# Performance work log

Hardware: AMD Instinct MI355X
Metric: run time of the kernel (lower is better)

The kernel has to match this reference:

```python
import jax, jax.numpy as jnp
import numpy as np

D = 1024
H = 16
HD = D // H

def setup_inputs() -> dict:
    key = jax.random.key(0)
    ks = jax.random.split(key, 8)
    scale = 1.0 / np.sqrt(D)
    x = jax.random.normal(ks[0], (2, 2048, D), dtype=jnp.float32)
    Wq = jax.random.uniform(ks[1], (D, D), jnp.float32, -scale, scale)
    bq = jax.random.uniform(ks[2], (D,), jnp.float32, -scale, scale)
    Wk = jax.random.uniform(ks[3], (D, D), jnp.float32, -scale, scale)
    bk = jax.random.uniform(ks[4], (D,), jnp.float32, -scale, scale)
    Wv = jax.random.uniform(ks[5], (D, D), jnp.float32, -scale, scale)
    bv = jax.random.uniform(ks[6], (D,), jnp.float32, -scale, scale)
    B = jnp.zeros((1, H, 1, 1), dtype=jnp.float32)
    return {"x": x, "Wq": Wq, "bq": bq, "Wk": Wk, "bk": bk, "Wv": Wv, "bv": bv, "B": B}

def reference(x, Wq, bq, Wk, bk, Wv, bv, B):
    bsz, seq, _ = x.shape
    def proj(W, b):
        # [b, s, D] -> [b, h, s, hd]
        y = x @ W.T + b
        return y.reshape(bsz, seq, H, HD).transpose(0, 2, 1, 3)
    q = proj(Wq, bq)
    k = proj(Wk, bk)
    v = proj(Wv, bv)
    scores = jnp.einsum('bhqd,bhkd->bhqk', q, k) / np.sqrt(HD) + B
    attn = jax.nn.softmax(scores, axis=-1)
    out = jnp.einsum('bhqk,bhkd->bhqd', attn, v)
    return out.transpose(0, 2, 1, 3).reshape(bsz, seq, D)
```

## Files before the change

kernel.cpp:

```cpp
#include <hip/hip_runtime.h>
#include <stdint.h>

typedef __attribute__((ext_vector_type(8))) short s8v;
typedef __attribute__((ext_vector_type(4))) short s4v;
typedef __attribute__((ext_vector_type(4))) float f4v;
typedef __attribute__((ext_vector_type(16))) float f16v;

#define D_DIM 1024
#define H_NUM 16
#define HD 64
#define SEQ 2048
#define BSZ 2
#define MROWS (BSZ * SEQ)
#define LOG2E 1.4426950408889634f

__device__ __forceinline__ unsigned short f2bf(float f) {
  unsigned u = __builtin_bit_cast(unsigned, f);
  u += 0x7fffu + ((u >> 16) & 1u);
  return (unsigned short)(u >> 16);
}

__device__ __forceinline__ float exp2q(float x) {
  float r;
  asm("v_exp_f32 %0, %1" : "=v"(r) : "v"(x));
  return r;
}

__device__ __forceinline__ float max3q(float a, float b, float c) {
  float r;
  asm("v_max3_f32 %0, %1, %2, %3" : "=v"(r) : "v"(a), "v"(b), "v"(c));
  return r;
}

__device__ __forceinline__ unsigned int cvtpk(float a, float b) {
  unsigned int r;
  asm("v_cvt_pk_bf16_f32 %0, %1, %2" : "=v"(r) : "v"(a), "v"(b));
  return r;
}

__device__ __forceinline__ void async16(const unsigned short* g, unsigned short* l) {
  __builtin_amdgcn_global_load_lds(
      (__attribute__((address_space(1))) unsigned int*)(uintptr_t)g,
      (__attribute__((address_space(3))) unsigned int*)l, 16, 0, 0);
}

__device__ __forceinline__ f4v mfma16(s8v a, s8v b, f4v c) {
  return __builtin_amdgcn_mfma_f32_16x16x32_bf16(a, b, c, 0, 0, 0);
}

__device__ __forceinline__ f16v mfma32(s8v a, s8v b, f16v c) {
  return __builtin_amdgcn_mfma_f32_32x32x16_bf16(a, b, c, 0, 0, 0);
}

__device__ __forceinline__ void barrier_raw() {
  __builtin_amdgcn_sched_barrier(0);
  __builtin_amdgcn_s_barrier();
  __builtin_amdgcn_sched_barrier(0);
}
#define WAITVM0() asm volatile("s_waitcnt vmcnt(0)" ::: "memory")

__global__ __launch_bounds__(256) void cvt_all(
    const float* __restrict__ x, const float* __restrict__ Wq,
    const float* __restrict__ Wk, const float* __restrict__ Wv,
    unsigned short* __restrict__ Xb, unsigned short* __restrict__ Wb) {
  const int NX = MROWS * D_DIM / 4;
  const int NW = D_DIM * D_DIM / 4;
  int i = blockIdx.x * 256 + threadIdx.x;
  const float* src;
  unsigned short* dst;
  int off;
  if (i < NX) {
    src = x; dst = Xb; off = i;
  } else if (i < NX + NW) {
    src = Wq; dst = Wb; off = i - NX;
  } else if (i < NX + 2 * NW) {
    src = Wk; dst = Wb + D_DIM * D_DIM; off = i - NX - NW;
  } else {
    src = Wv; dst = Wb + 2 * D_DIM * D_DIM; off = i - NX - 2 * NW;
  }
  f4v v = *(const f4v*)(src + (size_t)off * 4);
  s4v o;
  o[0] = (short)f2bf(v[0]);
  o[1] = (short)f2bf(v[1]);
  o[2] = (short)f2bf(v[2]);
  o[3] = (short)f2bf(v[3]);
  *(s4v*)(dst + (size_t)off * 4) = o;
}

__global__ __launch_bounds__(256) void qkv_gemm(
    const unsigned short* __restrict__ Xb, const unsigned short* __restrict__ Wb,
    const float* __restrict__ bq, const float* __restrict__ bk,
    const float* __restrict__ bv, unsigned short* __restrict__ qb,
    unsigned short* __restrict__ kb, unsigned short* __restrict__ vt) {
  __shared__ __align__(16) unsigned short At[2][128 * 32];
  __shared__ __align__(16) unsigned short Bt[2][128 * 32];

  const int z = blockIdx.z;
  const unsigned short* W = Wb + z * (D_DIM * D_DIM);
  const float* bias = (z == 0) ? bq : ((z == 1) ? bk : bv);
  const int row0 = blockIdx.x * 128;
  const int col0 = blockIdx.y * 128;
  const int t = threadIdx.x;
  const int w = t >> 6, l = t & 63;
  const int wr = w >> 1, wc = w & 1;
  const int lg = l >> 4, lc = l & 15;

  f4v acc[4][4];
#pragma unroll
  for (int m = 0; m < 4; ++m)
#pragma unroll
    for (int n = 0; n < 4; ++n) acc[m][n] = (f4v){0.f, 0.f, 0.f, 0.f};

  const int srow = t >> 2;
  const int sch = (t & 3) ^ ((t >> 3) & 3);
  const unsigned short* Asrc = Xb + (size_t)(row0 + srow) * D_DIM + sch * 8;
  const unsigned short* Bsrc = W + (size_t)(col0 + srow) * D_DIM + sch * 8;

  const int rch = lg ^ ((lc >> 1) & 3);
  const int arow = wr * 64 + lc;
  const int brow = wc * 64 + lc;

#define STAGE(b, k0)                                                        \
  do {                                                                      \
    async16(Asrc + (k0), At[b] + t * 8);                                    \
    async16(Asrc + (k0) + 64 * D_DIM, At[b] + 2048 + t * 8);                \
    async16(Bsrc + (k0), Bt[b] + t * 8);                                    \
    async16(Bsrc + (k0) + 64 * D_DIM, Bt[b] + 2048 + t * 8);                \
  } while (0)

  STAGE(0, 0);
  WAITVM0();
  barrier_raw();

  int cur = 0;
  for (int it = 0; it < 32; ++it) {
    if (it < 31) STAGE(cur ^ 1, (it + 1) * 32);
    s8v a[4], b[4];
#pragma unroll
    for (int m = 0; m < 4; ++m)
      a[m] = *(const s8v*)(At[cur] + (arow + m * 16) * 32 + rch * 8);
#pragma unroll
    for (int n = 0; n < 4; ++n)
      b[n] = *(const s8v*)(Bt[cur] + (brow + n * 16) * 32 + rch * 8);
    __builtin_amdgcn_s_setprio(1);
#pragma unroll
    for (int m = 0; m < 4; ++m)
#pragma unroll
      for (int n = 0; n < 4; ++n) acc[m][n] = mfma16(a[m], b[n], acc[m][n]);
    __builtin_amdgcn_s_setprio(0);
    WAITVM0();
    barrier_raw();
    cur ^= 1;
  }
#undef STAGE

  const float SCQ = 0.125f * LOG2E;
#pragma unroll
  for (int m = 0; m < 4; ++m) {
    const int sg0 = row0 + wr * 64 + m * 16 + 4 * lg;
    const int b = sg0 >> 11;
    const int sl0 = sg0 & (SEQ - 1);
#pragma unroll
    for (int n = 0; n < 4; ++n) {
      const int j = col0 + wc * 64 + n * 16 + lc;
      const int h = j >> 6, hd = j & 63;
      const float bs = bias[j];
      if (z == 2) {
        s4v o;
#pragma unroll
        for (int r = 0; r < 4; ++r) o[r] = (short)f2bf(acc[m][n][r] + bs);
        *(s4v*)(vt + ((size_t)(b * H_NUM + h) * HD + hd) * SEQ + sl0) = o;
      } else if (z == 0) {
#pragma unroll
        for (int r = 0; r < 4; ++r)
          qb[((size_t)(b * H_NUM + h) * SEQ + (sl0 + r)) * HD + hd] =
              f2bf((acc[m][n][r] + bs) * SCQ);
      } else {
#pragma unroll
        for (int r = 0; r < 4; ++r)
          kb[((size_t)(b * H_NUM + h) * SEQ + (sl0 + r)) * HD + hd] =
              f2bf(acc[m][n][r] + bs);
      }
    }
  }
}

__global__ __launch_bounds__(512, 4) void attn_fwd(
    const unsigned short* __restrict__ qb, const unsigned short* __restrict__ kb,
    const unsigned short* __restrict__ vt, const float* __restrict__ Bb,
    float* __restrict__ out) {
  __shared__ __align__(16) unsigned short Kl[2][2][64 * 64];
  __shared__ __align__(16) unsigned short Vl[2][2][64 * 64];

  const int bh = blockIdx.x;
  const int b = bh >> 4, h = bh & 15;
  const int q0 = blockIdx.y * 128;
  const int t = threadIdx.x, w = t >> 6, l = t & 63;
  const int ql = l & 31, hi = l >> 5;
  const int g = w >> 2;
  const int pw = w & 3;
  (void)Bb;

  const unsigned short* Q = qb + (size_t)bh * SEQ * HD;
  const unsigned short* K = kb + (size_t)bh * SEQ * HD;
  const unsigned short* V = vt + (size_t)bh * HD * SEQ;

  const int qrow = q0 + pw * 32 + ql;
  const unsigned short* Qp = Q + (size_t)qrow * HD + 8 * hi;
  s8v qf[4];
#pragma unroll
  for (int ks = 0; ks < 4; ++ks) qf[ks] = *(const s8v*)(Qp + ks * 16);

  f16v zf;
#pragma unroll
  for (int i = 0; i < 16; ++i) zf[i] = 0.f;
  f16v acc0 = zf, acc1 = zf;
  float m = -3.0e38f, thr = -3.0e38f, lsum = 0.f;

  int off0[4], off1[4];
#pragma unroll
  for (int ks = 0; ks < 4; ++ks) {
    off0[ks] = ql * 64 + (((2 * ks + hi) ^ (ql & 7)) * 8);
    off1[ks] = off0[ks] + 2048;
  }

  const int tg = t & 255;
  const int srow = tg >> 3;
  const int sc8 = (tg & 7) ^ (srow & 7);
  const unsigned short* Kst = K + (size_t)(g * 1024 + srow) * HD + sc8 * 8;
  const unsigned short* Vst = V + (size_t)srow * SEQ + g * 1024 + sc8 * 8;
  unsigned short* Kd = &Kl[g][0][tg * 8];
  unsigned short* Vd = &Vl[g][0][tg * 8];
  const int ldsw = 64 * 64;

#define STAGE_KV(bsel)                                                      \
  do {                                                                      \
    async16(Kst, Kd + (bsel) * ldsw);                                       \
    async16(Kst + 32 * HD, Kd + (bsel) * ldsw + 2048);                      \
    async16(Vst, Vd + (bsel) * ldsw);                                       \
    async16(Vst + 32 * SEQ, Vd + (bsel) * ldsw + 2048);                     \
    Kst += 64 * HD;                                                         \
    Vst += 64;                                                              \
  } while (0)

  STAGE_KV(0);
  WAITVM0();
  barrier_raw();

  int cur = 0;
  for (int kt = 0; kt < 16; ++kt) {
    if (kt < 15) STAGE_KV(cur ^ 1);

    const unsigned short* Kb_ = &Kl[g][cur][0];
    const unsigned short* Vb_ = &Vl[g][cur][0];

    f16v s0, s1;
    __builtin_amdgcn_s_setprio(1);
    {
      s8v kf0 = *(const s8v*)(Kb_ + off0[0]);
      s8v kf1 = *(const s8v*)(Kb_ + off1[0]);
      s0 = mfma32(kf0, qf[0], zf);
      s1 = mfma32(kf1, qf[0], zf);
    }
#pragma unroll
    for (int ks = 1; ks < 4; ++ks) {
      s8v kf0 = *(const s8v*)(Kb_ + off0[ks]);
      s8v kf1 = *(const s8v*)(Kb_ + off1[ks]);
      s0 = mfma32(kf0, qf[ks], s0);
      s1 = mfma32(kf1, qf[ks], s1);
    }
    __builtin_amdgcn_s_setprio(0);

    float a0 = max3q(s0[0], s0[1], s0[2]);
    float a1 = max3q(s0[3], s0[4], s0[5]);
    float a2 = max3q(s0[6], s0[7], s0[8]);
    float a3 = max3q(s0[9], s0[10], s0[11]);
    float a4 = max3q(s0[12], s0[13], s0[14]);
    float a5 = max3q(s0[15], s1[0], s1[1]);
    float a6 = max3q(s1[2], s1[3], s1[4]);
    float a7 = max3q(s1[5], s1[6], s1[7]);
    float a8 = max3q(s1[8], s1[9], s1[10]);
    float a9 = max3q(s1[11], s1[12], s1[13]);
    float b0 = max3q(a0, a1, a2);
    float b1 = max3q(a3, a4, a5);
    float b2 = max3q(a6, a7, a8);
    float b3 = max3q(a9, s1[14], s1[15]);
    float tmax = fmaxf(fmaxf(b0, b1), fmaxf(b2, b3));

    if (!__all(tmax <= thr)) {
      float tr = fmaxf(tmax, __shfl_xor(tmax, 32));
      const float mn = fmaxf(m, tr);
      const float fs = exp2q(m - mn);
      m = mn;
      thr = mn + 8.0f;
#pragma unroll
      for (int i = 0; i < 16; ++i) { acc0[i] *= fs; acc1[i] *= fs; }
      lsum *= fs;
    }

#pragma unroll
    for (int i = 0; i < 16; ++i) {
      s0[i] = exp2q(s0[i] - m);
      s1[i] = exp2q(s1[i] - m);
    }
    {
      float p0 = (s0[0] + s0[1]) + (s0[2] + s0[3]);
      float p1 = (s0[4] + s0[5]) + (s0[6] + s0[7]);
      float p2 = (s0[8] + s0[9]) + (s0[10] + s0[11]);
      float p3 = (s0[12] + s0[13]) + (s0[14] + s0[15]);
      float p4 = (s1[0] + s1[1]) + (s1[2] + s1[3]);
      float p5 = (s1[4] + s1[5]) + (s1[6] + s1[7]);
      float p6 = (s1[8] + s1[9]) + (s1[10] + s1[11]);
      float p7 = (s1[12] + s1[13]) + (s1[14] + s1[15]);
      lsum += ((p0 + p1) + (p2 + p3)) + ((p4 + p5) + (p6 + p7));
    }

    unsigned int u[16];
#pragma unroll
    for (int x = 0; x < 8; ++x) {
      u[x] = cvtpk(s0[2 * x], s0[2 * x + 1]);
      u[8 + x] = cvtpk(s1[2 * x], s1[2 * x + 1]);
    }
    s8v pb[4];
#pragma unroll
    for (int ks = 0; ks < 4; ++ks) {
      const int base = (ks >> 1) * 8 + (ks & 1) * 4;
      unsigned int x0 = u[base + 0], y0 = u[base + 2];
      unsigned int x1 = u[base + 1], y1 = u[base + 3];
      asm("v_permlane32_swap_b32 %0, %1" : "+v"(x0), "+v"(y0));
      asm("v_permlane32_swap_b32 %0, %1" : "+v"(x1), "+v"(y1));
      union { s8v v; unsigned int w[4]; } bb;
      bb.w[0] = x0; bb.w[1] = x1; bb.w[2] = y0; bb.w[3] = y1;
      pb[ks] = bb.v;
    }

    __builtin_amdgcn_s_setprio(1);
#pragma unroll
    for (int ks = 0; ks < 4; ++ks) {
      s8v vf0 = *(const s8v*)(Vb_ + off0[ks]);
      s8v vf1 = *(const s8v*)(Vb_ + off1[ks]);
      acc0 = mfma32(vf0, pb[ks], acc0);
      acc1 = mfma32(vf1, pb[ks], acc1);
    }
    __builtin_amdgcn_s_setprio(0);

    WAITVM0();
    barrier_raw();
    cur ^= 1;
  }
#undef STAGE_KV

  lsum += __shfl_xor(lsum, 32);

  float* exch = (float*)&Kl[0][0][0];
  float* mlb = (float*)&Vl[0][0][0];

  __syncthreads();
  if (g == 1) {
    float* dst = exch + ((size_t)(pw * 64 + l)) * 32;
#pragma unroll
    for (int gg = 0; gg < 4; ++gg) {
      f4v v0, v1;
#pragma unroll
      for (int r = 0; r < 4; ++r) { v0[r] = acc0[4 * gg + r]; v1[r] = acc1[4 * gg + r]; }
      *(f4v*)(dst + 4 * gg) = v0;
      *(f4v*)(dst + 16 + 4 * gg) = v1;
    }
    if (hi == 0) {
      mlb[pw * 32 + ql] = m;
      mlb[128 + pw * 32 + ql] = lsum;
    }
  }
  __syncthreads();
  if (g == 0) {
    const float mb = mlb[pw * 32 + ql];
    const float lb = mlb[128 + pw * 32 + ql];
    const float ms = fmaxf(m, mb);
    const float fa = exp2q(m - ms);
    const float fb = exp2q(mb - ms);
    const float linv = 1.0f / (lsum * fa + lb * fb);
    const float* src = exch + ((size_t)(pw * 64 + l)) * 32;
    const int q = q0 + pw * 32 + ql;
    float* op = out + ((size_t)(b * SEQ + q)) * D_DIM + h * 64;
#pragma unroll
    for (int gg = 0; gg < 4; ++gg) {
      f4v pa = *(const f4v*)(src + 4 * gg);
      f4v pc = *(const f4v*)(src + 16 + 4 * gg);
      f4v o0, o1;
#pragma unroll
      for (int r = 0; r < 4; ++r) {
        o0[r] = (acc0[4 * gg + r] * fa + pa[r] * fb) * linv;
        o1[r] = (acc1[4 * gg + r] * fa + pc[r] * fb) * linv;
      }
      *(f4v*)(op + 8 * gg + 4 * hi) = o0;
      *(f4v*)(op + 32 + 8 * gg + 4 * hi) = o1;
    }
  }
}

extern "C" void kernel_launch(void* const* d_in, const int* in_sizes, int n_in,
                              void* d_out, int out_size, void* d_ws, size_t ws_size,
                              hipStream_t stream) {
  const float* x = (const float*)d_in[0];
  const float* Wq = (const float*)d_in[1];
  const float* bq = (const float*)d_in[2];
  const float* Wk = (const float*)d_in[3];
  const float* bk = (const float*)d_in[4];
  const float* Wv = (const float*)d_in[5];
  const float* bv = (const float*)d_in[6];
  const float* Bb = (const float*)d_in[7];
  float* out = (float*)d_out;

  char* ws = (char*)d_ws;
  unsigned short* Xb = (unsigned short*)ws;
  unsigned short* Wb = (unsigned short*)(ws + (8ull << 20));
  unsigned short* qb = (unsigned short*)(ws + (14ull << 20));
  unsigned short* kb = (unsigned short*)(ws + (22ull << 20));
  unsigned short* vt = (unsigned short*)(ws + (30ull << 20));

  cvt_all<<<7168, 256, 0, stream>>>(x, Wq, Wk, Wv, Xb, Wb);

  dim3 ggrid(MROWS / 128, D_DIM / 128, 3);
  qkv_gemm<<<ggrid, 256, 0, stream>>>(Xb, Wb, bq, bk, bv, qb, kb, vt);

  dim3 agrid(BSZ * H_NUM, SEQ / 128);
  attn_fwd<<<agrid, 512, 0, stream>>>(qb, kb, vt, Bb, out);
}
```

Measured before the change: 95.02 us.

## Prefetch two KV tiles ahead with partial vmcnt waits in attention loop

The attention loop now issues the first two K/V tile loads before entering the loop. Each iteration waits with vmcnt(4), so only the current tile must have landed and the next tile stays in flight. The refill of a buffer is issued only after a trailing barrier, once that buffer has been consumed. The cross-group exchange buffer is relaid out slot-major to avoid LDS bank conflicts, and the final merge folds the normalization into two scale factors. This adds an extra barrier per iteration in exchange for deeper overlap of global loads with compute.

```diff
diff --git a/kernel.cpp b/kernel.cpp
--- a/kernel.cpp
+++ b/kernel.cpp
@@ -58,6 +58,7 @@
   __builtin_amdgcn_sched_barrier(0);
 }
 #define WAITVM0() asm volatile("s_waitcnt vmcnt(0)" ::: "memory")
+#define WAITVM4() asm volatile("s_waitcnt vmcnt(4)" ::: "memory")
 
 __global__ __launch_bounds__(256) void cvt_all(
     const float* __restrict__ x, const float* __restrict__ Wq,
@@ -244,15 +245,15 @@
   } while (0)
 
   STAGE_KV(0);
-  WAITVM0();
-  barrier_raw();
-
-  int cur = 0;
+  STAGE_KV(1);
+
   for (int kt = 0; kt < 16; ++kt) {
-    if (kt < 15) STAGE_KV(cur ^ 1);
-
-    const unsigned short* Kb_ = &Kl[g][cur][0];
-    const unsigned short* Vb_ = &Vl[g][cur][0];
+    if (kt < 15) WAITVM4();
+    else WAITVM0();
+    barrier_raw();
+
+    const unsigned short* Kb_ = &Kl[g][kt & 1][0];
+    const unsigned short* Vb_ = &Vl[g][kt & 1][0];
 
     f16v s0, s1;
     __builtin_amdgcn_s_setprio(1);
@@ -344,9 +345,8 @@
     }
     __builtin_amdgcn_s_setprio(0);
 
-    WAITVM0();
     barrier_raw();
-    cur ^= 1;
+    if (kt < 14) STAGE_KV(kt & 1);
   }
 #undef STAGE_KV
 
@@ -354,17 +354,17 @@
 
   float* exch = (float*)&Kl[0][0][0];
   float* mlb = (float*)&Vl[0][0][0];
+  const int slot = pw * 64 + l;
 
   __syncthreads();
   if (g == 1) {
-    float* dst = exch + ((size_t)(pw * 64 + l)) * 32;
 #pragma unroll
     for (int gg = 0; gg < 4; ++gg) {
       f4v v0, v1;
 #pragma unroll
       for (int r = 0; r < 4; ++r) { v0[r] = acc0[4 * gg + r]; v1[r] = acc1[4 * gg + r]; }
-      *(f4v*)(dst + 4 * gg) = v0;
-      *(f4v*)(dst + 16 + 4 * gg) = v1;
+      *(f4v*)(exch + (gg * 256 + slot) * 4) = v0;
+      *(f4v*)(exch + ((4 + gg) * 256 + slot) * 4) = v1;
     }
     if (hi == 0) {
       mlb[pw * 32 + ql] = m;
@@ -379,18 +379,18 @@
     const float fa = exp2q(m - ms);
     const float fb = exp2q(mb - ms);
     const float linv = 1.0f / (lsum * fa + lb * fb);
-    const float* src = exch + ((size_t)(pw * 64 + l)) * 32;
+    const float sa = fa * linv, sb = fb * linv;
     const int q = q0 + pw * 32 + ql;
     float* op = out + ((size_t)(b * SEQ + q)) * D_DIM + h * 64;
 #pragma unroll
     for (int gg = 0; gg < 4; ++gg) {
-      f4v pa = *(const f4v*)(src + 4 * gg);
-      f4v pc = *(const f4v*)(src + 16 + 4 * gg);
+      f4v pa = *(const f4v*)(exch + (gg * 256 + slot) * 4);
+      f4v pc = *(const f4v*)(exch + ((4 + gg) * 256 + slot) * 4);
       f4v o0, o1;
 #pragma unroll
       for (int r = 0; r < 4; ++r) {
-        o0[r] = (acc0[4 * gg + r] * fa + pa[r] * fb) * linv;
-        o1[r] = (acc1[4 * gg + r] * fa + pc[r] * fb) * linv;
+        o0[r] = acc0[4 * gg + r] * sa + pa[r] * sb;
+        o1[r] = acc1[4 * gg + r] * sa + pc[r] * sb;
       }
       *(f4v*)(op + 8 * gg + 4 * hi) = o0;
       *(f4v*)(op + 32 + 8 * gg + 4 * hi) = o1;
```

After: 93.69 us. No clear change (-1.4%).
